# Performance work log

Hardware: AMD Instinct MI355X
Metric: run time of the kernel (lower is better)

The kernel has to match this reference:

```python
import jax, jax.numpy as jnp
import numpy as np

HID = 512
NHEADS = 8
HEAD_DIM = HID // NHEADS  # 64
L = 2048
B = 4
LQ = 128
SCALE = float(np.sqrt(HEAD_DIM))


def _xavier(k, shape):
    lim = float(np.sqrt(6.0 / (shape[0] + shape[1])))
    return jax.random.uniform(k, shape, jnp.float32, -lim, lim)


def setup_inputs() -> dict:
    key = jax.random.key(0)
    ks = jax.random.split(key, 9)
    query = jax.random.normal(ks[0], (L, B, HID), jnp.float32)
    key_t = jax.random.normal(ks[1], (L, B, HID), jnp.float32)
    value = jax.random.normal(ks[2], (L, B, HID), jnp.float32)
    # 1 = pad, 0 = valid (code adds (1-mask).log() to scores)
    key_padding_mask = jax.random.bernoulli(ks[3], 0.1, (B, L)).astype(jnp.float32)
    question_rel_emb = jax.random.normal(ks[4], (LQ, LQ, B, HID), jnp.float32) * 0.02
    Wq = _xavier(ks[5], (HID, HID))
    Wk = _xavier(ks[6], (HID, HID))
    Wv = _xavier(ks[7], (HID, HID))
    Wo = _xavier(ks[8], (HID, HID))
    return dict(query=query, key_t=key_t, value=value,
                key_padding_mask=key_padding_mask,
                question_rel_emb=question_rel_emb,
                Wq=Wq, Wk=Wk, Wv=Wv, Wo=Wo)


def reference(query, key_t, value, key_padding_mask, question_rel_emb, Wq, Wk, Wv, Wo):
    # head_reshape: [L,B,HID] -> [B*K, L, D] (b outer, k inner, matching torch view)
    def heads(x, W):
        y = x @ W.T                                   # [L,B,HID]
        return jnp.swapaxes(y.reshape(L, B * NHEADS, HEAD_DIM), 0, 1)

    q = heads(query, Wq)    # [BK,L,D]
    k = heads(key_t, Wk)
    v = heads(value, Wv)

    attn = jnp.einsum('nld,nmd->nlm', q, k)            # [BK,L,L]

    # question relative bias: proj_key over [Lq,Lq,B,HID] -> [BK,Lq,Lq,D]
    qr = question_rel_emb @ Wk.T
    qr = qr.reshape(LQ, LQ, B * NHEADS, HEAD_DIM).transpose(2, 0, 1, 3)
    bias = jnp.einsum('nijd,nid->nij', qr, q[:, -LQ:])  # [BK,Lq,Lq]
    attn = attn.at[:, -LQ:, -LQ:].add(bias)

    attn = attn / SCALE

    # padding mask: repeat_interleave over batch, add log(1-mask) per key column
    kpm = jnp.repeat(key_padding_mask, NHEADS, axis=0)  # [BK,L]
    attn = attn + jnp.log1p(-kpm)[:, None, :]

    attn = jax.nn.softmax(attn, axis=-1)
    out = jnp.einsum('nlm,nmd->nld', attn, v)           # [BK,L,D]
    out = jnp.swapaxes(out, 0, 1).reshape(L, B, HID) @ Wo.T
    return (out, attn)
```

## Files before the change

kernel.cpp:

```cpp
#include <hip/hip_runtime.h>
#include <hip/hip_bf16.h>


using short8   = __attribute__((ext_vector_type(8))) short;
using short4v  = __attribute__((ext_vector_type(4))) short;
using ushort4v = __attribute__((ext_vector_type(4))) unsigned short;
using f32x4    = __attribute__((ext_vector_type(4))) float;

#define L_T   2048
#define B_T   4
#define HID_T 512
#define HD_T  64
#define LQ_T  128
#define L0_T  1920

__device__ __forceinline__ float b2f(unsigned short u){
  return __uint_as_float(((unsigned int)u) << 16);
}
__device__ __forceinline__ unsigned short f2b(float f){
  unsigned int u = __float_as_uint(f);
  u += 0x7FFFu + ((u >> 16) & 1u);
  return (unsigned short)(u >> 16);
}
__device__ __forceinline__ f32x4 mfma16(short8 a, short8 b, f32x4 c){
  return __builtin_amdgcn_mfma_f32_16x16x32_bf16(a, b, c, 0, 0, 0);
}
#if __has_builtin(__builtin_amdgcn_mfma_f32_16x16x16bf16_1k)
__device__ __forceinline__ f32x4 mfma16k16(short4v a, short4v b, f32x4 c){
  return __builtin_amdgcn_mfma_f32_16x16x16bf16_1k(a, b, c, 0, 0, 0);
}
#else
__device__ __forceinline__ f32x4 mfma16k16(short4v a, short4v b, f32x4 c){
  f32x4 d;
  asm("v_mfma_f32_16x16x16_bf16 %0, %1, %2, %0"
      : "=v"(d) : "v"(a), "v"(b), "0"(c));
  return d;
}
#endif

__global__ __launch_bounds__(256) void k_splitW(const float* __restrict__ w0,
                                                const float* __restrict__ w1,
                                                const float* __restrict__ w2,
                                                const float* __restrict__ w3,
                                                unsigned short* __restrict__ hi,
                                                unsigned short* __restrict__ lo)
{
  int wid = blockIdx.y;
  const float* src = (wid == 0) ? w0 : (wid == 1) ? w1 : (wid == 2) ? w2 : w3;
  int chunk = blockIdx.x * 256 + threadIdx.x;
  int o = chunk >> 7;
  int hpos = (chunk & 127) * 4;
  f32x4 v = ((const f32x4*)src)[chunk];
  ushort4v h4, l4;
  #pragma unroll
  for (int e = 0; e < 4; e++){
    unsigned short h = f2b(v[e]);
    h4[e] = h;
    l4[e] = f2b(v[e] - b2f(h));
  }
  size_t idx = ((size_t)(wid * 512 + (o >> 4) * 16 + (hpos >> 5))) * 512
             + (((hpos & 31) >> 3) * 16 + (o & 15)) * 8 + (hpos & 7);
  *(ushort4v*)(hi + idx) = h4;
  *(ushort4v*)(lo + idx) = l4;
}

__global__ __launch_bounds__(256) void k_proj3(const float* __restrict__ Xq,
                                               const float* __restrict__ Xk,
                                               const float* __restrict__ Xv,
                                               const unsigned short* __restrict__ WhA,
                                               const unsigned short* __restrict__ WlA,
                                               unsigned short* __restrict__ qhp,
                                               unsigned short* __restrict__ qlp,
                                               unsigned short* __restrict__ khp,
                                               unsigned short* __restrict__ klp,
                                               unsigned short* __restrict__ vpk)
{
  int sel = blockIdx.x >> 10;
  int bx  = blockIdx.x & 1023;
  const float* X = (sel == 0) ? Xq : (sel == 1) ? Xk : Xv;
  const short* WH = (const short*)WhA + (size_t)sel * 262144;
  const short* WL = (const short*)WlA + (size_t)sel * 262144;
  unsigned short* ohi = (sel == 0) ? qhp : khp;
  unsigned short* olo = (sel == 0) ? qlp : klp;

  int wv = threadIdx.x >> 6, lane = threadIdx.x & 63;
  int tid = bx * 4 + wv;
  int mt = tid >> 3, nt = tid & 7;
  int row0 = mt * 16, col0 = nt * 64;
  int lhi = lane >> 4, llo = lane & 15;
  int arow = row0 + llo;
  f32x4 acc[4] = {{0,0,0,0},{0,0,0,0},{0,0,0,0},{0,0,0,0}};
  #pragma unroll 4
  for (int k0 = 0; k0 < 512; k0 += 32){
    const float* ap = X + (size_t)arow * 512 + k0 + lhi * 8;
    f32x4 a01 = *(const f32x4*)ap;
    f32x4 a23 = *(const f32x4*)(ap + 4);
    short8 ah, al;
    #pragma unroll
    for (int e = 0; e < 4; e++){
      unsigned short h0 = f2b(a01[e]);
      ah[e] = (short)h0;  al[e] = (short)f2b(a01[e] - b2f(h0));
      unsigned short h1 = f2b(a23[e]);
      ah[e + 4] = (short)h1;  al[e + 4] = (short)f2b(a23[e] - b2f(h1));
    }
    int kk = k0 >> 5;
    #pragma unroll
    for (int cb = 0; cb < 4; cb++){
      size_t bidx = (size_t)(((col0 >> 4) + cb) * 16 + kk) * 512 + lane * 8;
      short8 bh = *(const short8*)(WH + bidx);
      short8 bl = *(const short8*)(WL + bidx);
      acc[cb] = mfma16(ah, bh, acc[cb]);
      acc[cb] = mfma16(al, bh, acc[cb]);
      acc[cb] = mfma16(ah, bl, acc[cb]);
    }
  }
  #pragma unroll
  for (int cb = 0; cb < 4; cb++){
    #pragma unroll
    for (int r = 0; r < 4; r++){
      int row = row0 + lhi * 4 + r;
      int o   = col0 + cb * 16 + llo;
      int l = row >> 2, bb = row & 3;
      int n = bb * 8 + (o >> 6), d = o & 63;
      float v = acc[cb][r];
      if (sel != 2){
        size_t idx = ((size_t)(n * 128 + (l >> 4)) * 2 + (d >> 5)) * 512
                   + (((d & 31) >> 3) * 16 + (l & 15)) * 8 + (d & 7);
        unsigned short h = f2b(v);
        ohi[idx] = h;
        olo[idx] = f2b(v - b2f(h));
      } else {
        int m = l;
        size_t idx = (((size_t)(n * 128 + (m >> 4)) * 4) + (d >> 4)) * 256
                   + ((m & 15) >> 2) * 64 + (d & 15) * 4 + (m & 3);
        vpk[idx] = f2b(v);
      }
    }
  }
}

__global__ __launch_bounds__(256) void k_tb(const unsigned short* __restrict__ qhp,
                                            const unsigned short* __restrict__ qlp,
                                            const float* __restrict__ Wk,
                                            const float* __restrict__ qrem,
                                            float* __restrict__ bias)
{
  int bb = blockIdx.x & 3, i = blockIdx.x >> 2;
  __shared__ float qv[8][64];
  __shared__ float ts[8][512];
  for (int idx = threadIdx.x; idx < 512; idx += 256){
    int kh = idx >> 6, d = idx & 63;
    int n = bb * 8 + kh;
    int row = L0_T + i;
    size_t qidx = ((size_t)(n * 128 + (row >> 4)) * 2 + (d >> 5)) * 512
                + (((d & 31) >> 3) * 16 + (row & 15)) * 8 + (d & 7);
    qv[kh][d] = b2f(qhp[qidx]) + b2f(qlp[qidx]);
  }
  __syncthreads();
  {
    int kh = threadIdx.x >> 5, h0 = (threadIdx.x & 31) * 16;
    f32x4 a0 = {0,0,0,0}, a1 = {0,0,0,0}, a2 = {0,0,0,0}, a3 = {0,0,0,0};
    for (int d = 0; d < 64; d++){
      float qd = qv[kh][d];
      const float* wr = Wk + (size_t)(kh * 64 + d) * 512 + h0;
      a0 += qd * *(const f32x4*)(wr);
      a1 += qd * *(const f32x4*)(wr + 4);
      a2 += qd * *(const f32x4*)(wr + 8);
      a3 += qd * *(const f32x4*)(wr + 12);
    }
    *(f32x4*)&ts[kh][h0]      = a0;
    *(f32x4*)&ts[kh][h0 + 4]  = a1;
    *(f32x4*)&ts[kh][h0 + 8]  = a2;
    *(f32x4*)&ts[kh][h0 + 12] = a3;
  }
  __syncthreads();
  int wv = threadIdx.x >> 6, lane = threadIdx.x & 63;
  for (int j = wv; j < 128; j += 4){
    const float* qr = qrem + (((size_t)i * LQ_T + j) * B_T + bb) * 512;
    f32x4 v0 = *(const f32x4*)(qr + lane * 4);
    f32x4 v1 = *(const f32x4*)(qr + 256 + lane * 4);
    float pl[8];
    #pragma unroll
    for (int kh = 0; kh < 8; kh++){
      f32x4 t0 = *(const f32x4*)&ts[kh][lane * 4];
      f32x4 t1 = *(const f32x4*)&ts[kh][256 + lane * 4];
      pl[kh] = v0[0]*t0[0] + v0[1]*t0[1] + v0[2]*t0[2] + v0[3]*t0[3]
             + v1[0]*t1[0] + v1[1]*t1[1] + v1[2]*t1[2] + v1[3]*t1[3];
    }
    #pragma unroll
    for (int kh = 0; kh < 8; kh++){
      float s = pl[kh];
      #pragma unroll
      for (int msk = 1; msk < 64; msk <<= 1) s += __shfl_xor(s, msk);
      pl[kh] = s;
    }
    if (lane == 0){
      #pragma unroll
      for (int kh = 0; kh < 8; kh++)
        bias[((size_t)(bb * 8 + kh) * LQ_T + i) * LQ_T + j] = pl[kh];
    }
  }
}

__attribute__((amdgpu_waves_per_eu(2, 2)))
__global__ __launch_bounds__(512) void k_attn(
    const unsigned short* __restrict__ qhp, const unsigned short* __restrict__ qlp,
    const unsigned short* __restrict__ khp, const unsigned short* __restrict__ klp,
    const float* __restrict__ bias, const float* __restrict__ kpm,
    const unsigned short* __restrict__ vpk,
    float* __restrict__ attnF, float* __restrict__ outbk)
{
  __shared__ __attribute__((aligned(16))) float pf[8 * 1024];
  __shared__ float2 red2[2 * 128];
  const int w = threadIdx.x >> 6, lane = threadIdx.x & 63;
  const int lhi = lane >> 4, llo = lane & 15;

  for (int j = 0; j < 8; ++j){
    const int p = blockIdx.x + (j << 8);
    const int n = p >> 6, rbp = p & 63;
    const int rbA = rbp * 2, rbB = rbA + 1;
    const int row0A = rbA * 16, row0B = rbB * 16, bb = n >> 3;

    const short* QHA = (const short*)qhp + ((size_t)(n * 128 + rbA) * 2) * 512 + lane * 8;
    const short* QLA = (const short*)qlp + ((size_t)(n * 128 + rbA) * 2) * 512 + lane * 8;
    const short* QHB = (const short*)qhp + ((size_t)(n * 128 + rbB) * 2) * 512 + lane * 8;
    const short* QLB = (const short*)qlp + ((size_t)(n * 128 + rbB) * 2) * 512 + lane * 8;
    short8 qhA0 = *(const short8*)(QHA);
    short8 qhA1 = *(const short8*)(QHA + 512);
    short8 qlA0 = *(const short8*)(QLA);
    short8 qlA1 = *(const short8*)(QLA + 512);
    short8 qhB0 = *(const short8*)(QHB);
    short8 qhB1 = *(const short8*)(QHB + 512);
    short8 qlB0 = *(const short8*)(QLB);
    short8 qlB1 = *(const short8*)(QLB + 512);
    const short* KH = (const short*)khp + (size_t)n * 131072 + w * 1024 + lane * 8;
    const short* KL = (const short*)klp + (size_t)n * 131072 + w * 1024 + lane * 8;

    float svA[16][4], svB[16][4];
    #pragma unroll
    for (int t = 0; t < 16; t++){
      short8 kh0v = *(const short8*)(KH + t * 8192);
      short8 kh1v = *(const short8*)(KH + t * 8192 + 512);
      short8 kl0v = *(const short8*)(KL + t * 8192);
      short8 kl1v = *(const short8*)(KL + t * 8192 + 512);
      f32x4 aA = {0.f, 0.f, 0.f, 0.f};
      f32x4 aB = {0.f, 0.f, 0.f, 0.f};
      aA = mfma16(kh0v, qhA0, aA);
      aA = mfma16(kl0v, qhA0, aA);
      aA = mfma16(kh0v, qlA0, aA);
      aA = mfma16(kh1v, qhA1, aA);
      aA = mfma16(kl1v, qhA1, aA);
      aA = mfma16(kh1v, qlA1, aA);
      aB = mfma16(kh0v, qhB0, aB);
      aB = mfma16(kl0v, qhB0, aB);
      aB = mfma16(kh0v, qlB0, aB);
      aB = mfma16(kh1v, qhB1, aB);
      aB = mfma16(kl1v, qhB1, aB);
      aB = mfma16(kh1v, qlB1, aB);
      if (t == 15 && rbp >= 60){
        int j0 = w * 16 + lhi * 4;
        int iA = row0A - L0_T + llo;
        int iB = row0B - L0_T + llo;
        aA += *(const f32x4*)(bias + ((size_t)(n * 128 + iA)) * 128 + j0);
        aB += *(const f32x4*)(bias + ((size_t)(n * 128 + iB)) * 128 + j0);
      }
      f32x4 mkv = *(const f32x4*)(kpm + bb * 2048 + (w + t * 8) * 16 + lhi * 4);
      #pragma unroll
      for (int r = 0; r < 4; r++){
        float mk = (mkv[r] != 0.f) ? -__builtin_inff() : 0.f;
        svA[t][r] = aA[r] * 0.125f + mk;
        svB[t][r] = aB[r] * 0.125f + mk;
      }
    }

    float pmA = svA[0][0], pmB = svB[0][0];
    #pragma unroll
    for (int t = 0; t < 16; t++)
      #pragma unroll
      for (int r = 0; r < 4; r++){
        pmA = fmaxf(pmA, svA[t][r]);
        pmB = fmaxf(pmB, svB[t][r]);
      }
    pmA = fmaxf(pmA, __shfl_xor(pmA, 16));
    pmA = fmaxf(pmA, __shfl_xor(pmA, 32));
    pmB = fmaxf(pmB, __shfl_xor(pmB, 16));
    pmB = fmaxf(pmB, __shfl_xor(pmB, 32));
    float esA = 0.f, esB = 0.f;
    #pragma unroll
    for (int t = 0; t < 16; t++)
      #pragma unroll
      for (int r = 0; r < 4; r++){
        float eA = __expf(svA[t][r] - pmA);
        float eB = __expf(svB[t][r] - pmB);
        svA[t][r] = eA;  esA += eA;
        svB[t][r] = eB;  esB += eB;
      }
    esA += __shfl_xor(esA, 16);
    esA += __shfl_xor(esA, 32);
    esB += __shfl_xor(esB, 16);
    esB += __shfl_xor(esB, 32);
    if (lane < 16){
      red2[w * 16 + llo]       = make_float2(pmA, esA);
      red2[128 + w * 16 + llo] = make_float2(pmB, esB);
    }
    asm volatile("s_waitcnt lgkmcnt(0)\n\ts_barrier" ::: "memory");

    float facA, facB;
    {
      float2 c0 = red2[(lhi * 2 + 0) * 16 + llo];
      float2 c1 = red2[(lhi * 2 + 1) * 16 + llo];
      float mg = fmaxf(c0.x, c1.x);
      mg = fmaxf(mg, __shfl_xor(mg, 16));
      mg = fmaxf(mg, __shfl_xor(mg, 32));
      float cg = c0.y * __expf(c0.x - mg) + c1.y * __expf(c1.x - mg);
      cg += __shfl_xor(cg, 16);
      cg += __shfl_xor(cg, 32);
      facA = __expf(pmA - mg) / cg;
    }
    {
      float2 c0 = red2[128 + (lhi * 2 + 0) * 16 + llo];
      float2 c1 = red2[128 + (lhi * 2 + 1) * 16 + llo];
      float mg = fmaxf(c0.x, c1.x);
      mg = fmaxf(mg, __shfl_xor(mg, 16));
      mg = fmaxf(mg, __shfl_xor(mg, 32));
      float cg = c0.y * __expf(c0.x - mg) + c1.y * __expf(c1.x - mg);
      cg += __shfl_xor(cg, 16);
      cg += __shfl_xor(cg, 32);
      facB = __expf(pmB - mg) / cg;
    }

    float* aRowA = attnF + ((size_t)(n * L_T + row0A + llo)) * L_T;
    float* aRowB = attnF + ((size_t)(n * L_T + row0B + llo)) * L_T;
    const short* VP = (const short*)vpk + (size_t)n * 131072 + w * 1024 + lane * 4;
    f32x4 pA0 = {0,0,0,0}, pA1 = {0,0,0,0}, pA2 = {0,0,0,0}, pA3 = {0,0,0,0};
    f32x4 pB0 = {0,0,0,0}, pB1 = {0,0,0,0}, pB2 = {0,0,0,0}, pB3 = {0,0,0,0};
    #pragma unroll
    for (int t = 0; t < 16; t++){
      short4v v0 = *(const short4v*)(VP + t * 8192 +   0);
      short4v v1 = *(const short4v*)(VP + t * 8192 + 256);
      short4v v2 = *(const short4v*)(VP + t * 8192 + 512);
      short4v v3 = *(const short4v*)(VP + t * 8192 + 768);
      f32x4 pvA, pvB;
      #pragma unroll
      for (int r = 0; r < 4; r++){
        pvA[r] = svA[t][r] * facA;
        pvB[r] = svB[t][r] * facB;
      }
      __builtin_nontemporal_store(pvA, (f32x4*)(aRowA + (w + t * 8) * 16 + lhi * 4));
      __builtin_nontemporal_store(pvB, (f32x4*)(aRowB + (w + t * 8) * 16 + lhi * 4));
      short4v pbA, pbB;
      #pragma unroll
      for (int r = 0; r < 4; r++){
        pbA[r] = (short)f2b(pvA[r]);
        pbB[r] = (short)f2b(pvB[r]);
      }
      pA0 = mfma16k16(v0, pbA, pA0);
      pA1 = mfma16k16(v1, pbA, pA1);
      pA2 = mfma16k16(v2, pbA, pA2);
      pA3 = mfma16k16(v3, pbA, pA3);
      pB0 = mfma16k16(v0, pbB, pB0);
      pB1 = mfma16k16(v1, pbB, pB1);
      pB2 = mfma16k16(v2, pbB, pB2);
      pB3 = mfma16k16(v3, pbB, pB3);
    }

    float* pfw = pf + w * 1024 + llo * 64;
    *(f32x4*)(pfw + (( 0 + lhi * 4 + llo * 4) & 63)) = pA0;
    *(f32x4*)(pfw + ((16 + lhi * 4 + llo * 4) & 63)) = pA1;
    *(f32x4*)(pfw + ((32 + lhi * 4 + llo * 4) & 63)) = pA2;
    *(f32x4*)(pfw + ((48 + lhi * 4 + llo * 4) & 63)) = pA3;
    asm volatile("s_waitcnt lgkmcnt(0)\n\ts_barrier" ::: "memory");
    {
      int d = lane;
      int q = w;
      int slot = (d + q * 4) & 63;
      float s = 0.f;
      #pragma unroll
      for (int ww = 0; ww < 8; ww++) s += pf[ww * 1024 + q * 64 + slot];
      outbk[((size_t)(n * L_T + row0A + q)) * HD_T + d] = s;
      int q2 = w + 8;
      int slot2 = (d + q2 * 4) & 63;
      float s2 = 0.f;
      #pragma unroll
      for (int ww = 0; ww < 8; ww++) s2 += pf[ww * 1024 + q2 * 64 + slot2];
      outbk[((size_t)(n * L_T + row0A + q2)) * HD_T + d] = s2;
    }
    asm volatile("s_waitcnt lgkmcnt(0)\n\ts_barrier" ::: "memory");
    *(f32x4*)(pfw + (( 0 + lhi * 4 + llo * 4) & 63)) = pB0;
    *(f32x4*)(pfw + ((16 + lhi * 4 + llo * 4) & 63)) = pB1;
    *(f32x4*)(pfw + ((32 + lhi * 4 + llo * 4) & 63)) = pB2;
    *(f32x4*)(pfw + ((48 + lhi * 4 + llo * 4) & 63)) = pB3;
    asm volatile("s_waitcnt lgkmcnt(0)\n\ts_barrier" ::: "memory");
    {
      int d = lane;
      int q = w;
      int slot = (d + q * 4) & 63;
      float s = 0.f;
      #pragma unroll
      for (int ww = 0; ww < 8; ww++) s += pf[ww * 1024 + q * 64 + slot];
      outbk[((size_t)(n * L_T + row0B + q)) * HD_T + d] = s;
      int q2 = w + 8;
      int slot2 = (d + q2 * 4) & 63;
      float s2 = 0.f;
      #pragma unroll
      for (int ww = 0; ww < 8; ww++) s2 += pf[ww * 1024 + q2 * 64 + slot2];
      outbk[((size_t)(n * L_T + row0B + q2)) * HD_T + d] = s2;
    }
  }
}

__global__ __launch_bounds__(256) void k_final(const float* __restrict__ outbk,
                                               const unsigned short* __restrict__ Wh,
                                               const unsigned short* __restrict__ Wl,
                                               float* __restrict__ y)
{
  int wv = threadIdx.x >> 6, lane = threadIdx.x & 63;
  int tid = blockIdx.x * 4 + wv;
  int mt = tid >> 5, nt = tid & 31;
  int row0 = mt * 16, col0 = nt * 16;
  int lhi = lane >> 4, llo = lane & 15;
  int arow = row0 + llo;
  int l = arow >> 2, bb = arow & 3;
  const short* WHs = (const short*)Wh;
  const short* WLs = (const short*)Wl;
  f32x4 acc = {0.f, 0.f, 0.f, 0.f};
  for (int k0 = 0; k0 < 512; k0 += 32){
    int c = k0 + lhi * 8;
    const float* ap = outbk + ((size_t)(bb * 8 + (c >> 6)) * L_T + l) * HD_T + (c & 63);
    f32x4 a01 = *(const f32x4*)ap;
    f32x4 a23 = *(const f32x4*)(ap + 4);
    short8 ahi, alo;
    #pragma unroll
    for (int e = 0; e < 4; e++){
      unsigned short h0 = f2b(a01[e]);
      ahi[e] = (short)h0;  alo[e] = (short)f2b(a01[e] - b2f(h0));
      unsigned short h1 = f2b(a23[e]);
      ahi[e + 4] = (short)h1;  alo[e + 4] = (short)f2b(a23[e] - b2f(h1));
    }
    size_t bidx = (size_t)(nt * 16 + (k0 >> 5)) * 512 + lane * 8;
    short8 bh = *(const short8*)(WHs + bidx);
    short8 bl = *(const short8*)(WLs + bidx);
    acc = mfma16(ahi, bh, acc);
    acc = mfma16(alo, bh, acc);
    acc = mfma16(ahi, bl, acc);
  }
  #pragma unroll
  for (int r = 0; r < 4; r++)
    y[(size_t)(row0 + lhi * 4 + r) * 512 + col0 + llo] = acc[r];
}

extern "C" void kernel_launch(void* const* d_in, const int* in_sizes, int n_in,
                              void* d_out, int out_size, void* d_ws, size_t ws_size,
                              hipStream_t stream)
{
  const float* query = (const float*)d_in[0];
  const float* key_t = (const float*)d_in[1];
  const float* value = (const float*)d_in[2];
  const float* kpm   = (const float*)d_in[3];
  const float* qrem  = (const float*)d_in[4];
  const float* Wq    = (const float*)d_in[5];
  const float* Wk    = (const float*)d_in[6];
  const float* Wv    = (const float*)d_in[7];
  const float* Wo    = (const float*)d_in[8];

  float* outY  = (float*)d_out;
  float* attnF = outY + (size_t)L_T * B_T * HID_T;

  char* wp = (char*)d_ws;
  const size_t SZ8M = (size_t)32 * 2048 * 64 * 2;
  unsigned short* qhp = (unsigned short*)wp; wp += SZ8M;
  unsigned short* qlp = (unsigned short*)wp; wp += SZ8M;
  unsigned short* khp = (unsigned short*)wp; wp += SZ8M;
  unsigned short* klp = (unsigned short*)wp; wp += SZ8M;
  unsigned short* vpk = (unsigned short*)wp; wp += SZ8M;
  unsigned short* whA = (unsigned short*)wp; wp += (size_t)4 * 512 * 512 * 2;
  unsigned short* wlA = (unsigned short*)wp; wp += (size_t)4 * 512 * 512 * 2;
  float* biasb = (float*)wp; wp += (size_t)32 * 128 * 128 * 4;
  float* outbk = (float*)wp; wp += (size_t)32 * 2048 * 64 * 4;

  const size_t WSTEP = (size_t)512 * 512;

  k_splitW<<<dim3(256, 4), 256, 0, stream>>>(Wq, Wk, Wv, Wo, whA, wlA);
  k_proj3<<<3072, 256, 0, stream>>>(query, key_t, value, whA, wlA,
                                    qhp, qlp, khp, klp, vpk);
  k_tb<<<512, 256, 0, stream>>>(qhp, qlp, Wk, qrem, biasb);
  k_attn<<<256, 512, 0, stream>>>(qhp, qlp, khp, klp, biasb, kpm,
                                  vpk, attnF, outbk);
  k_final<<<4096, 256, 0, stream>>>(outbk, whA + 3 * WSTEP, wlA + 3 * WSTEP, outY);
}
```

Measured before the change: 470.0 us.

## Stream K tiles through triple-buffered LDS via async global_load_lds

The per-iteration direct global loads of the K hi/lo fragments are replaced by asynchronous global-to-LDS copies into a per-wave triple buffer, issued two tiles ahead and fenced with explicit vmcnt waits. The aim is to hide global-memory latency behind the MFMA work of the score loop and to free vector registers. In exchange it adds about 96KB of shared memory per block, extra LDS reads, and hand-counted waitcnt values that must stay consistent with the other global loads in the loop.

```diff
diff --git a/kernel.cpp b/kernel.cpp
--- a/kernel.cpp
+++ b/kernel.cpp
@@ -210,6 +210,7 @@
     const unsigned short* __restrict__ vpk,
     float* __restrict__ attnF, float* __restrict__ outbk)
 {
+  __shared__ __attribute__((aligned(16))) short kvb[8][3][4][512];
   __shared__ __attribute__((aligned(16))) float pf[8 * 1024];
   __shared__ float2 red2[2 * 128];
   const int w = threadIdx.x >> 6, lane = threadIdx.x & 63;
@@ -236,13 +237,40 @@
     const short* KH = (const short*)khp + (size_t)n * 131072 + w * 1024 + lane * 8;
     const short* KL = (const short*)klp + (size_t)n * 131072 + w * 1024 + lane * 8;
 
+    #define STAGE_K(tt, bq) do {                                               \
+      __builtin_amdgcn_global_load_lds(                                        \
+        (const __attribute__((address_space(1))) unsigned int*)(KH + (tt) * 8192),        \
+        (__attribute__((address_space(3))) unsigned int*)&kvb[w][bq][0][0], 16, 0, 0);    \
+      __builtin_amdgcn_global_load_lds(                                        \
+        (const __attribute__((address_space(1))) unsigned int*)(KH + (tt) * 8192 + 512),  \
+        (__attribute__((address_space(3))) unsigned int*)&kvb[w][bq][1][0], 16, 0, 0);    \
+      __builtin_amdgcn_global_load_lds(                                        \
+        (const __attribute__((address_space(1))) unsigned int*)(KL + (tt) * 8192),        \
+        (__attribute__((address_space(3))) unsigned int*)&kvb[w][bq][2][0], 16, 0, 0);    \
+      __builtin_amdgcn_global_load_lds(                                        \
+        (const __attribute__((address_space(1))) unsigned int*)(KL + (tt) * 8192 + 512),  \
+        (__attribute__((address_space(3))) unsigned int*)&kvb[w][bq][3][0], 16, 0, 0);    \
+    } while (0)
+
+    STAGE_K(0, 0);
+    STAGE_K(1, 1);
+
     float svA[16][4], svB[16][4];
     #pragma unroll
     for (int t = 0; t < 16; t++){
-      short8 kh0v = *(const short8*)(KH + t * 8192);
-      short8 kh1v = *(const short8*)(KH + t * 8192 + 512);
-      short8 kl0v = *(const short8*)(KL + t * 8192);
-      short8 kl1v = *(const short8*)(KL + t * 8192 + 512);
+      const int cur = t % 3;
+      if (t < 14){
+        STAGE_K(t + 2, ((t + 2) % 3));
+        asm volatile("s_waitcnt vmcnt(8)" ::: "memory");
+      } else if (t == 14){
+        asm volatile("s_waitcnt vmcnt(4)" ::: "memory");
+      } else {
+        asm volatile("s_waitcnt vmcnt(0)" ::: "memory");
+      }
+      short8 kh0v = *(const short8*)&kvb[w][cur][0][lane * 8];
+      short8 kh1v = *(const short8*)&kvb[w][cur][1][lane * 8];
+      short8 kl0v = *(const short8*)&kvb[w][cur][2][lane * 8];
+      short8 kl1v = *(const short8*)&kvb[w][cur][3][lane * 8];
       f32x4 aA = {0.f, 0.f, 0.f, 0.f};
       f32x4 aB = {0.f, 0.f, 0.f, 0.f};
       aA = mfma16(kh0v, qhA0, aA);
@@ -272,6 +300,7 @@
         svB[t][r] = aB[r] * 0.125f + mk;
       }
     }
+    #undef STAGE_K
 
     float pmA = svA[0][0], pmB = svB[0][0];
     #pragma unroll
```

Measured after the change: 506.2 us. 7.7% more time.

## Stage bf16-split input rows in shared memory for reuse across projection waves

Applied to the files above, without the earlier changes.

The QKV projection kernel now loads a block's 16 input rows once, splits them into hi/lo bf16 in shared memory, and has each of four waves compute two 64-column tiles from that shared copy. Before, every wave re-read its fp32 rows from global memory and redid the split for its own column tile, so each row was fetched and converted eight times. The grid is halved to 1536 blocks. Shared-memory use rises and there are fewer waves per launch, which may lower occupancy.

```diff
diff --git a/kernel.cpp b/kernel.cpp
--- a/kernel.cpp
+++ b/kernel.cpp
@@ -75,65 +75,80 @@
                                                unsigned short* __restrict__ klp,
                                                unsigned short* __restrict__ vpk)
 {
-  int sel = blockIdx.x >> 10;
-  int bx  = blockIdx.x & 1023;
+  __shared__ short ahl[16][520];
+  __shared__ short all_[16][520];
+  int sel = blockIdx.x >> 9;
+  int mt  = blockIdx.x & 511;
   const float* X = (sel == 0) ? Xq : (sel == 1) ? Xk : Xv;
   const short* WH = (const short*)WhA + (size_t)sel * 262144;
   const short* WL = (const short*)WlA + (size_t)sel * 262144;
   unsigned short* ohi = (sel == 0) ? qhp : khp;
   unsigned short* olo = (sel == 0) ? qlp : klp;
 
+  #pragma unroll
+  for (int i = 0; i < 8; i++){
+    int c = threadIdx.x + 256 * i;
+    int row = c >> 7;
+    int k4  = (c & 127) * 4;
+    f32x4 v = *(const f32x4*)(X + (size_t)(mt * 16 + row) * 512 + k4);
+    ushort4v h4, l4;
+    #pragma unroll
+    for (int e = 0; e < 4; e++){
+      unsigned short h = f2b(v[e]);
+      h4[e] = h;
+      l4[e] = f2b(v[e] - b2f(h));
+    }
+    int kk = k4 >> 5;
+    int slot = (((k4 & 31) >> 3) * 16 + row) * 8 + (k4 & 7);
+    *(ushort4v*)&ahl[kk][slot]  = h4;
+    *(ushort4v*)&all_[kk][slot] = l4;
+  }
+  __syncthreads();
+
   int wv = threadIdx.x >> 6, lane = threadIdx.x & 63;
-  int tid = bx * 4 + wv;
-  int mt = tid >> 3, nt = tid & 7;
-  int row0 = mt * 16, col0 = nt * 64;
   int lhi = lane >> 4, llo = lane & 15;
-  int arow = row0 + llo;
-  f32x4 acc[4] = {{0,0,0,0},{0,0,0,0},{0,0,0,0},{0,0,0,0}};
-  #pragma unroll 4
-  for (int k0 = 0; k0 < 512; k0 += 32){
-    const float* ap = X + (size_t)arow * 512 + k0 + lhi * 8;
-    f32x4 a01 = *(const f32x4*)ap;
-    f32x4 a23 = *(const f32x4*)(ap + 4);
-    short8 ah, al;
-    #pragma unroll
-    for (int e = 0; e < 4; e++){
-      unsigned short h0 = f2b(a01[e]);
-      ah[e] = (short)h0;  al[e] = (short)f2b(a01[e] - b2f(h0));
-      unsigned short h1 = f2b(a23[e]);
-      ah[e + 4] = (short)h1;  al[e + 4] = (short)f2b(a23[e] - b2f(h1));
-    }
-    int kk = k0 >> 5;
+  int row0 = mt * 16;
+
+  #pragma unroll
+  for (int half = 0; half < 2; half++){
+    int ntl = wv * 2 + half;
+    int col0 = ntl * 64;
+    f32x4 acc[4] = {{0,0,0,0},{0,0,0,0},{0,0,0,0},{0,0,0,0}};
+    #pragma unroll 4
+    for (int kk = 0; kk < 16; kk++){
+      short8 ah = *(const short8*)&ahl[kk][lane * 8];
+      short8 al = *(const short8*)&all_[kk][lane * 8];
+      #pragma unroll
+      for (int cb = 0; cb < 4; cb++){
+        size_t bidx = (size_t)(((col0 >> 4) + cb) * 16 + kk) * 512 + lane * 8;
+        short8 bh = *(const short8*)(WH + bidx);
+        short8 bl = *(const short8*)(WL + bidx);
+        acc[cb] = mfma16(ah, bh, acc[cb]);
+        acc[cb] = mfma16(al, bh, acc[cb]);
+        acc[cb] = mfma16(ah, bl, acc[cb]);
+      }
+    }
     #pragma unroll
     for (int cb = 0; cb < 4; cb++){
-      size_t bidx = (size_t)(((col0 >> 4) + cb) * 16 + kk) * 512 + lane * 8;
-      short8 bh = *(const short8*)(WH + bidx);
-      short8 bl = *(const short8*)(WL + bidx);
-      acc[cb] = mfma16(ah, bh, acc[cb]);
-      acc[cb] = mfma16(al, bh, acc[cb]);
-      acc[cb] = mfma16(ah, bl, acc[cb]);
-    }
-  }
-  #pragma unroll
-  for (int cb = 0; cb < 4; cb++){
-    #pragma unroll
-    for (int r = 0; r < 4; r++){
-      int row = row0 + lhi * 4 + r;
-      int o   = col0 + cb * 16 + llo;
-      int l = row >> 2, bb = row & 3;
-      int n = bb * 8 + (o >> 6), d = o & 63;
-      float v = acc[cb][r];
-      if (sel != 2){
-        size_t idx = ((size_t)(n * 128 + (l >> 4)) * 2 + (d >> 5)) * 512
-                   + (((d & 31) >> 3) * 16 + (l & 15)) * 8 + (d & 7);
-        unsigned short h = f2b(v);
-        ohi[idx] = h;
-        olo[idx] = f2b(v - b2f(h));
-      } else {
-        int m = l;
-        size_t idx = (((size_t)(n * 128 + (m >> 4)) * 4) + (d >> 4)) * 256
-                   + ((m & 15) >> 2) * 64 + (d & 15) * 4 + (m & 3);
-        vpk[idx] = f2b(v);
+      #pragma unroll
+      for (int r = 0; r < 4; r++){
+        int row = row0 + lhi * 4 + r;
+        int o   = col0 + cb * 16 + llo;
+        int l = row >> 2, bb = row & 3;
+        int n = bb * 8 + (o >> 6), d = o & 63;
+        float v = acc[cb][r];
+        if (sel != 2){
+          size_t idx = ((size_t)(n * 128 + (l >> 4)) * 2 + (d >> 5)) * 512
+                     + (((d & 31) >> 3) * 16 + (l & 15)) * 8 + (d & 7);
+          unsigned short h = f2b(v);
+          ohi[idx] = h;
+          olo[idx] = f2b(v - b2f(h));
+        } else {
+          int m = l;
+          size_t idx = (((size_t)(n * 128 + (m >> 4)) * 4) + (d >> 4)) * 256
+                     + ((m & 15) >> 2) * 64 + (d & 15) * 4 + (m & 3);
+          vpk[idx] = f2b(v);
+        }
       }
     }
   }
@@ -481,7 +496,7 @@
   const size_t WSTEP = (size_t)512 * 512;
 
   k_splitW<<<dim3(256, 4), 256, 0, stream>>>(Wq, Wk, Wv, Wo, whA, wlA);
-  k_proj3<<<3072, 256, 0, stream>>>(query, key_t, value, whA, wlA,
+  k_proj3<<<1536, 256, 0, stream>>>(query, key_t, value, whA, wlA,
                                     qhp, qlp, khp, klp, vpk);
   k_tb<<<512, 256, 0, stream>>>(qhp, qlp, Wk, qrem, biasb);
   k_attn<<<256, 512, 0, stream>>>(qhp, qlp, khp, klp, biasb, kpm,
```

Result: no change. 461.0 us (-1.9%).
